# Performance work log

Measured on AMD Instinct MI355X. Metric: run time of the kernel, lower is better.

Reference implementation:

```python
import math
import jax, jax.numpy as jnp
import numpy as np

B, L, D, H = 4, 1024, 512, 8
DK = D // H

def setup_inputs() -> dict:
    key = jax.random.key(0)
    ks = jax.random.split(key, 12)
    s = 0.02
    return {
        "query": jax.random.normal(ks[0], (B, L, D), jnp.float32),
        "key": jax.random.normal(ks[1], (B, L, D), jnp.float32),
        "value": jax.random.normal(ks[2], (B, L, D), jnp.float32),
        "wq_w": jax.random.normal(ks[3], (D, D), jnp.float32) * s,
        "wq_b": jnp.zeros((D,), jnp.float32),
        "wk_w": jax.random.normal(ks[4], (D, D), jnp.float32) * s,
        "wk_b": jnp.zeros((D,), jnp.float32),
        "wv_w": jax.random.normal(ks[5], (D, D), jnp.float32) * s,
        "wv_b": jnp.zeros((D,), jnp.float32),
        "dense_w": jax.random.normal(ks[6], (D, D), jnp.float32) * s,
        "dense_b": jnp.zeros((D,), jnp.float32),
        "gate_w": jax.random.normal(ks[7], (D, 1), jnp.float32) * s,
        "gate_b": jnp.zeros((1,), jnp.float32),
        "mp_wq_w": jax.random.normal(ks[8], (D, D), jnp.float32) * s,
        "mp_wq_b": jnp.zeros((D,), jnp.float32),
        "mp_wk_w": jax.random.normal(ks[9], (D, D), jnp.float32) * s,
        "mp_wk_b": jnp.zeros((D,), jnp.float32),
    }

def reference(query, key, value, wq_w, wq_b, wk_w, wk_b, wv_w, wv_b,
              dense_w, dense_b, gate_w, gate_b,
              mp_wq_w, mp_wq_b, mp_wk_w, mp_wk_b):
    # Multi-head projections -> (B, H, L, DK)
    q = (query @ wq_w + wq_b).reshape(B, L, H, DK).transpose(0, 2, 1, 3)
    k = (key @ wk_w + wk_b).reshape(B, L, H, DK).transpose(0, 2, 1, 3)
    v = (value @ wv_w + wv_b).reshape(B, L, H, DK).transpose(0, 2, 1, 3)

    # MaskPerturbation on original (unprojected-into-heads) Q, K; scale by sqrt(d_model)
    qp = query @ mp_wq_w + mp_wq_b              # (B, L, D)
    kp = key @ mp_wk_w + mp_wk_b                # (B, L, D)
    m = jax.nn.sigmoid(jnp.einsum('bqd,bkd->bqk', qp, kp) / math.sqrt(D))  # (B, L, L)

    # Scaled dot-product attention (no mask)
    scores = jnp.einsum('bhqd,bhkd->bhqk', q, k) / math.sqrt(DK)  # (B, H, L, L)
    p_attn = jax.nn.softmax(scores, axis=-1)

    # Calibration: attn_cal = attn * exp(1 - m), combined with per-query gate, re-softmax
    attn_cal = p_attn * jnp.exp(1.0 - m[:, None])                 # (B, H, L, L)
    g = jax.nn.sigmoid(query @ gate_w + gate_b)[:, None]          # (B, 1, L, 1)
    attn_comb = g * p_attn + (1.0 - g) * attn_cal
    attn_final = jax.nn.softmax(attn_comb, axis=-1)

    out = jnp.einsum('bhqk,bhkd->bhqd', attn_final, v)            # (B, H, L, DK)
    out = out.transpose(0, 2, 1, 3).reshape(B, L, D)
    out = out @ dense_w + dense_b                                 # dropout p=0 (eval)
    return (out, m)
```

## Files before the change

### kernel.cpp

```cpp
#include <hip/hip_runtime.h>

#define B_  4
#define L_  1024
#define D_  512
#define H_  8
#define DK_ 64
#define BL_ (B_*L_)

typedef unsigned short us16;
typedef __attribute__((ext_vector_type(8))) short bf16x8;
typedef __attribute__((ext_vector_type(4))) float f32x4;

__device__ __forceinline__ float us2f(us16 u) {
  union { unsigned int i; float f; } x;
  x.i = ((unsigned int)u) << 16;
  return x.f;
}
__device__ __forceinline__ us16 f2us(float f) {
  union { float f; unsigned int i; } x;
  x.f = f;
  unsigned int r = x.i + 0x7FFFu + ((x.i >> 16) & 1u);
  return (us16)(r >> 16);
}
__device__ __forceinline__ us16 cvt_us(float f) { return f2us(f); }
__device__ __forceinline__ us16 cvt_us(us16 u) { return u; }
__device__ __forceinline__ float fexp2(float x) {
  return __builtin_amdgcn_exp2f(x);
}

#define MFMA(a, b, c) __builtin_amdgcn_mfma_f32_16x16x32_bf16(a, b, c, 0, 0, 0)

struct WT6 {
  const float* src[6];
  us16* dst[6];
};
__global__ __launch_bounds__(256) void wtrans6(WT6 p) {
  __shared__ us16 T[64][72];
  const int z = blockIdx.z;
  const float* __restrict__ W = p.src[z];
  us16* __restrict__ Wt = p.dst[z];
  const int t = threadIdx.x;
  const int k0 = blockIdx.y * 64, n0 = blockIdx.x * 64;
  {
    int r = t >> 2, c = (t & 3) * 16;
    const float* src = W + (size_t)(k0 + r) * 512 + n0 + c;
    union { bf16x8 v; us16 u[8]; } p0, p1;
#pragma unroll
    for (int j = 0; j < 8; ++j) { p0.u[j] = f2us(src[j]); p1.u[j] = f2us(src[8 + j]); }
    *(bf16x8*)&T[r][c] = p0.v;
    *(bf16x8*)&T[r][c + 8] = p1.v;
  }
  __syncthreads();
  {
    int n = t >> 2, c = (t & 3) * 16;
    union { bf16x8 v; us16 u[8]; } p0, p1;
#pragma unroll
    for (int j = 0; j < 8; ++j) { p0.u[j] = T[c + j][n]; p1.u[j] = T[c + 8 + j][n]; }
    us16* dst = Wt + (size_t)(n0 + n) * 512 + k0 + c;
    *(bf16x8*)dst = p0.v;
    *(bf16x8*)(dst + 8) = p1.v;
  }
}

struct GJob { const float* A; const us16* Wt; const float* bias; us16* C; int mode; };
struct GJobs { GJob j[3]; };

__global__ __launch_bounds__(256) void gemm3(GJobs jobs) {
  __shared__ us16 Al[64][72];
  __shared__ us16 Wl[64][72];
  int f = blockIdx.x + 8 * (blockIdx.y + 64 * blockIdx.z);
  const int cpx = 64 * (int)gridDim.z;
  f = (f & 7) * cpx + (f >> 3);
  const int bx = f & 7, by = (f >> 3) & 63, bz = f >> 9;
  const GJob J = jobs.j[bz];
  const int tid = threadIdx.x;
  const int w = tid >> 6, lane = tid & 63;
  const int quad = lane >> 4, lc = lane & 15;
  const int row0 = by * 64, col0 = bx * 64;
  const int sr = tid >> 2, sc = (tid & 3) * 16;
  f32x4 acc[4] = {};
  for (int k0 = 0; k0 < 512; k0 += 64) {
    {
      const float* as = J.A + (size_t)(row0 + sr) * 512 + k0 + sc;
      union { bf16x8 v; us16 u[8]; } p0, p1;
#pragma unroll
      for (int j = 0; j < 8; ++j) { p0.u[j] = f2us(as[j]); p1.u[j] = f2us(as[8 + j]); }
      *(bf16x8*)&Al[sr][sc] = p0.v;
      *(bf16x8*)&Al[sr][sc + 8] = p1.v;
    }
    {
      const us16* wsrc = J.Wt + (size_t)(col0 + sr) * 512 + k0 + sc;
      *(bf16x8*)&Wl[sr][sc] = *(const bf16x8*)wsrc;
      *(bf16x8*)&Wl[sr][sc + 8] = *(const bf16x8*)(wsrc + 8);
    }
    __syncthreads();
    bf16x8 a0 = *(const bf16x8*)&Al[w * 16 + lc][quad * 8];
    bf16x8 a1 = *(const bf16x8*)&Al[w * 16 + lc][32 + quad * 8];
#pragma unroll
    for (int ct = 0; ct < 4; ++ct) {
      bf16x8 b0 = *(const bf16x8*)&Wl[ct * 16 + lc][quad * 8];
      bf16x8 b1 = *(const bf16x8*)&Wl[ct * 16 + lc][32 + quad * 8];
      acc[ct] = MFMA(a0, b0, acc[ct]);
      acc[ct] = MFMA(a1, b1, acc[ct]);
    }
    __syncthreads();
  }
  const int orow = row0 + w * 16 + quad * 4;
#pragma unroll
  for (int ct = 0; ct < 4; ++ct) {
    const int col = col0 + ct * 16 + lc;
    const float bv = J.bias[col];
    if (J.mode == 0) {
#pragma unroll
      for (int r = 0; r < 4; ++r)
        J.C[(size_t)(orow + r) * 512 + col] = f2us(acc[ct][r] + bv);
    } else {
      const int h = col >> 6, dk = col & 63;
#pragma unroll
      for (int r = 0; r < 4; ++r) {
        const int grow = orow + r;
        const int b = grow >> 10, kv = grow & 1023;
        J.C[(((size_t)b * H_ + h) * DK_ + dk) * L_ + kv] = f2us(acc[ct][r] + bv);
      }
    }
  }
}

__global__ __launch_bounds__(256) void gemm_dense(
    const us16* __restrict__ A, const us16* __restrict__ Wt,
    const float* __restrict__ bias, float* __restrict__ C) {
  __shared__ us16 Al[64][72];
  __shared__ us16 Wl[64][72];
  int f = blockIdx.x + 8 * blockIdx.y;
  f = (f & 7) * 64 + (f >> 3);
  const int bx = f & 7, by = f >> 3;
  const int tid = threadIdx.x;
  const int w = tid >> 6, lane = tid & 63;
  const int quad = lane >> 4, lc = lane & 15;
  const int row0 = by * 64, col0 = bx * 64;
  const int sr = tid >> 2, sc = (tid & 3) * 16;
  f32x4 acc[4] = {};
  for (int k0 = 0; k0 < 512; k0 += 64) {
    const us16* as = A + (size_t)(row0 + sr) * 512 + k0 + sc;
    const us16* wsrc = Wt + (size_t)(col0 + sr) * 512 + k0 + sc;
    *(bf16x8*)&Al[sr][sc] = *(const bf16x8*)as;
    *(bf16x8*)&Al[sr][sc + 8] = *(const bf16x8*)(as + 8);
    *(bf16x8*)&Wl[sr][sc] = *(const bf16x8*)wsrc;
    *(bf16x8*)&Wl[sr][sc + 8] = *(const bf16x8*)(wsrc + 8);
    __syncthreads();
    bf16x8 a0 = *(const bf16x8*)&Al[w * 16 + lc][quad * 8];
    bf16x8 a1 = *(const bf16x8*)&Al[w * 16 + lc][32 + quad * 8];
#pragma unroll
    for (int ct = 0; ct < 4; ++ct) {
      bf16x8 b0 = *(const bf16x8*)&Wl[ct * 16 + lc][quad * 8];
      bf16x8 b1 = *(const bf16x8*)&Wl[ct * 16 + lc][32 + quad * 8];
      acc[ct] = MFMA(a0, b0, acc[ct]);
      acc[ct] = MFMA(a1, b1, acc[ct]);
    }
    __syncthreads();
  }
  const int orow = row0 + w * 16 + quad * 4;
#pragma unroll
  for (int ct = 0; ct < 4; ++ct) {
    const int col = col0 + ct * 16 + lc;
    const float bv = bias[col];
#pragma unroll
    for (int r = 0; r < 4; ++r)
      C[(size_t)(orow + r) * 512 + col] = acc[ct][r] + bv;
  }
}

__global__ __launch_bounds__(256) void gate_kernel(
    const float* __restrict__ query, const float* __restrict__ gw,
    const float* __restrict__ gb, float* __restrict__ g) {
  int row = blockIdx.x * 4 + (threadIdx.x >> 6);
  int lane = threadIdx.x & 63;
  float p = 0.f;
  for (int d = lane; d < D_; d += 64) p += query[(size_t)row * D_ + d] * gw[d];
#pragma unroll
  for (int off = 32; off; off >>= 1) p += __shfl_down(p, off);
  if (lane == 0) g[row] = 1.f / (1.f + __expf(-(p + gb[0])));
}

template <bool WK>
__global__ __launch_bounds__(256) void mask16(
    const us16* __restrict__ QP, const us16* __restrict__ KP,
    float* __restrict__ Mout, const float* __restrict__ gbuf,
    us16* __restrict__ Wk) {
  __shared__ us16 Al[64][56];
  __shared__ us16 Bl[64][56];
  int f = blockIdx.x + 16 * (blockIdx.y + 16 * blockIdx.z);
  f = (f & 7) * 128 + (f >> 3);
  const int bx = f & 15, by = (f >> 4) & 15, b = f >> 8;
  const int tid = threadIdx.x;
  const int w = tid >> 6, lane = tid & 63;
  const int quad = lane >> 4, lc = lane & 15;
  const int row0 = by * 64, col0 = bx * 64;
  const us16* Ab = QP + (size_t)b * L_ * D_;
  const us16* Bb = KP + (size_t)b * L_ * D_;
  f32x4 acc[4] = {};
  const int arow = tid >> 2, aks = (tid & 3) * 8;
  for (int k0 = 0; k0 < 512; k0 += 32) {
    *(bf16x8*)&Al[arow][aks] =
        *(const bf16x8*)(Ab + (size_t)(row0 + arow) * 512 + k0 + aks);
    *(bf16x8*)&Bl[arow][aks] =
        *(const bf16x8*)(Bb + (size_t)(col0 + arow) * 512 + k0 + aks);
    __syncthreads();
    bf16x8 af = *(const bf16x8*)&Al[w * 16 + lc][quad * 8];
#pragma unroll
    for (int ct = 0; ct < 4; ++ct) {
      bf16x8 bf = *(const bf16x8*)&Bl[ct * 16 + lc][quad * 8];
      acc[ct] = MFMA(af, bf, acc[ct]);
    }
    __syncthreads();
  }
  const float sc = 0.04419417382415922f;
  const int orow = row0 + w * 16 + quad * 4;
  float gq[4];
  if (WK) {
#pragma unroll
    for (int r = 0; r < 4; ++r) gq[r] = gbuf[b * L_ + orow + r];
  }
#pragma unroll
  for (int ct = 0; ct < 4; ++ct) {
    const int col = col0 + ct * 16 + lc;
#pragma unroll
    for (int r = 0; r < 4; ++r) {
      float x = acc[ct][r] * sc;
      float v = 1.f / (1.f + __expf(-x));
      size_t idx = ((size_t)b * L_ + orow + r) * L_ + col;
      Mout[idx] = v;
      if (WK) Wk[idx] = f2us(gq[r] + (1.f - gq[r]) * __expf(1.f - v));
    }
  }
}

__global__ __launch_bounds__(256, 4) void attn5(
    const us16* Qp, const us16* __restrict__ Kp,
    const us16* __restrict__ Vt, const us16* __restrict__ Wk, us16* O) {
  __shared__ us16 P[16 * 1032];
  __shared__ float red[2][4][16];
  const int tid = threadIdx.x;
  const int w = tid >> 6, lane = tid & 63;
  const int quad = lane >> 4, lc = lane & 15;
  int f = blockIdx.x + 64 * (blockIdx.y + 8 * blockIdx.z);
  f = (f & 7) * 256 + (f >> 3);
  const int q0 = (f & 63) * 16;
  const int h = (f >> 6) & 7;
  const int b = f >> 9;

  const us16* qptr = Qp + (size_t)(b * L_ + q0 + lc) * D_ + h * DK_;
  bf16x8 qa0 = *(const bf16x8*)(qptr + quad * 8);
  bf16x8 qa1 = *(const bf16x8*)(qptr + 32 + quad * 8);

  const us16* Kbase = Kp + (size_t)b * L_ * D_ + h * DK_;
  const float c1 = 0.18033688011112042f;

  float s[16][4];
  float sm[4] = {0.f, 0.f, 0.f, 0.f};
#pragma unroll
  for (int kt = 0; kt < 16; ++kt) {
    const us16* kr = Kbase + (size_t)(kt * 64 + w * 16 + lc) * D_;
    bf16x8 b0 = *(const bf16x8*)(kr + quad * 8);
    bf16x8 b1 = *(const bf16x8*)(kr + 32 + quad * 8);
    f32x4 a = {};
    __builtin_amdgcn_s_setprio(1);
    a = MFMA(qa0, b0, a);
    a = MFMA(qa1, b1, a);
    __builtin_amdgcn_s_setprio(0);
#pragma unroll
    for (int r = 0; r < 4; ++r) {
      float e = fexp2(a[r] * c1);
      s[kt][r] = e;
      sm[r] += e;
    }
  }
#pragma unroll
  for (int r = 0; r < 4; ++r)
#pragma unroll
    for (int off = 1; off < 16; off <<= 1) sm[r] += __shfl_xor(sm[r], off);
  if (lc == 0)
#pragma unroll
    for (int r = 0; r < 4; ++r) red[0][w][quad * 4 + r] = sm[r];
  __syncthreads();
  float invr[4];
#pragma unroll
  for (int r = 0; r < 4; ++r) {
    const int row = quad * 4 + r;
    invr[r] = 1.44269504088896341f /
              (red[0][0][row] + red[0][1][row] + red[0][2][row] + red[0][3][row]);
  }

  const us16* wkb = Wk + (size_t)(b * L_ + q0 + quad * 4) * L_ + w * 16 + lc;
  float ts[4] = {0.f, 0.f, 0.f, 0.f};
#pragma unroll
  for (int kt = 0; kt < 16; ++kt) {
#pragma unroll
    for (int r = 0; r < 4; ++r) {
      float cv = s[kt][r] * invr[r] * us2f(wkb[(size_t)r * L_ + kt * 64]);
      float e2 = fexp2(cv);
      ts[r] += e2;
      P[(quad * 4 + r) * 1032 + kt * 64 + w * 16 + lc] = f2us(e2);
    }
  }
#pragma unroll
  for (int r = 0; r < 4; ++r)
#pragma unroll
    for (int off = 1; off < 16; off <<= 1) ts[r] += __shfl_xor(ts[r], off);
  if (lc == 0)
#pragma unroll
    for (int r = 0; r < 4; ++r) red[1][w][quad * 4 + r] = ts[r];
  __syncthreads();

  const us16* Vb = Vt + ((size_t)(b * H_ + h) * DK_ + w * 16 + lc) * L_;
  f32x4 oacc = {};
  for (int kv = 0; kv < L_; kv += 32) {
    bf16x8 pa = *(const bf16x8*)&P[lc * 1032 + kv + quad * 8];
    bf16x8 vb = *(const bf16x8*)(Vb + kv + quad * 8);
    __builtin_amdgcn_s_setprio(1);
    oacc = MFMA(pa, vb, oacc);
    __builtin_amdgcn_s_setprio(0);
  }
#pragma unroll
  for (int r = 0; r < 4; ++r) {
    const int row = quad * 4 + r;
    float inv2 = 1.f /
        (red[1][0][row] + red[1][1][row] + red[1][2][row] + red[1][3][row]);
    O[(size_t)(b * L_ + q0 + row) * D_ + h * DK_ + w * 16 + lc] =
        f2us(oacc[r] * inv2);
  }
}

template <int MODE, typename TA>
__global__ __launch_bounds__(256) void gemm16(
    const TA* __restrict__ A, const float* __restrict__ W,
    const float* __restrict__ bias, void* __restrict__ Cout) {
  __shared__ us16 Al[64][56];
  __shared__ us16 Wl[64][56];
  const int tid = threadIdx.x;
  const int w = tid >> 6, lane = tid & 63;
  const int quad = lane >> 4, lc = lane & 15;
  const int row0 = blockIdx.y * 64, col0 = blockIdx.x * 64;
  f32x4 acc[4] = {};
  const int arow = tid >> 2, aks = (tid & 3) * 8;
  const int wk = tid & 31, wns = (tid >> 5) * 8;
  for (int k0 = 0; k0 < 512; k0 += 32) {
    {
      union { bf16x8 v; us16 u[8]; } pk;
      const TA* src = A + (size_t)(row0 + arow) * 512 + k0 + aks;
#pragma unroll
      for (int j = 0; j < 8; ++j) pk.u[j] = cvt_us(src[j]);
      *(bf16x8*)&Al[arow][aks] = pk.v;
    }
    {
      const float* src = W + (size_t)(k0 + wk) * 512 + col0 + wns;
#pragma unroll
      for (int j = 0; j < 8; ++j) Wl[wns + j][wk] = f2us(src[j]);
    }
    __syncthreads();
    bf16x8 af = *(const bf16x8*)&Al[w * 16 + lc][quad * 8];
#pragma unroll
    for (int ct = 0; ct < 4; ++ct) {
      bf16x8 bf = *(const bf16x8*)&Wl[ct * 16 + lc][quad * 8];
      acc[ct] = MFMA(af, bf, acc[ct]);
    }
    __syncthreads();
  }
  const int orow = row0 + w * 16 + quad * 4;
#pragma unroll
  for (int ct = 0; ct < 4; ++ct) {
    const int col = col0 + ct * 16 + lc;
    const float bv = bias[col];
    if (MODE == 0) {
      us16* C = (us16*)Cout;
#pragma unroll
      for (int r = 0; r < 4; ++r)
        C[(size_t)(orow + r) * 512 + col] = f2us(acc[ct][r] + bv);
    } else if (MODE == 1) {
      us16* C = (us16*)Cout;
      const int h = col >> 6, dk = col & 63;
#pragma unroll
      for (int r = 0; r < 4; ++r) {
        const int grow = orow + r;
        const int b = grow >> 10, kv = grow & 1023;
        C[(((size_t)b * H_ + h) * DK_ + dk) * L_ + kv] = f2us(acc[ct][r] + bv);
      }
    } else {
      float* C = (float*)Cout;
#pragma unroll
      for (int r = 0; r < 4; ++r)
        C[(size_t)(orow + r) * 512 + col] = acc[ct][r] + bv;
    }
  }
}

__global__ __launch_bounds__(256, 3) void attn2_fb(
    const us16* Qp, const us16* __restrict__ Kp,
    const us16* __restrict__ Vt, const float* __restrict__ Mm,
    const float* __restrict__ gbuf, us16* O) {
  __shared__ us16 Ql[16][72];
  __shared__ us16 P[16 * 1032];
  __shared__ float red[2][4][16];
  const int tid = threadIdx.x;
  const int w = tid >> 6, lane = tid & 63;
  const int quad = lane >> 4, lc = lane & 15;
  const int b = blockIdx.z, h = blockIdx.y, q0 = blockIdx.x * 16;
  if (tid < 128) {
    int r = tid >> 3, ks = (tid & 7) * 8;
    *(bf16x8*)&Ql[r][ks] =
        *(const bf16x8*)(Qp + (size_t)(b * L_ + q0 + r) * D_ + h * DK_ + ks);
  }
  __syncthreads();
  bf16x8 qa0 = *(const bf16x8*)&Ql[lc][quad * 8];
  bf16x8 qa1 = *(const bf16x8*)&Ql[lc][32 + quad * 8];
  const us16* Kbase = Kp + (size_t)b * L_ * D_ + h * DK_;
  float s[16][4];
#pragma unroll
  for (int kt = 0; kt < 16; ++kt) {
    const us16* kr = Kbase + (size_t)(kt * 64 + w * 16 + lc) * D_;
    bf16x8 b0 = *(const bf16x8*)(kr + quad * 8);
    bf16x8 b1 = *(const bf16x8*)(kr + 32 + quad * 8);
    f32x4 a = {};
    a = MFMA(qa0, b0, a);
    a = MFMA(qa1, b1, a);
#pragma unroll
    for (int r = 0; r < 4; ++r) s[kt][r] = a[r] * 0.125f;
  }
  float sm[4];
#pragma unroll
  for (int r = 0; r < 4; ++r) {
    float t = 0.f;
#pragma unroll
    for (int kt = 0; kt < 16; ++kt) { s[kt][r] = __expf(s[kt][r]); t += s[kt][r]; }
#pragma unroll
    for (int off = 1; off < 16; off <<= 1) t += __shfl_xor(t, off);
    sm[r] = t;
  }
  if (lc == 0)
#pragma unroll
    for (int r = 0; r < 4; ++r) red[0][w][quad * 4 + r] = sm[r];
  __syncthreads();
  float inv[4];
#pragma unroll
  for (int r = 0; r < 4; ++r) {
    const int row = quad * 4 + r;
    inv[r] = 1.f / (red[0][0][row] + red[0][1][row] + red[0][2][row] + red[0][3][row]);
  }
  float gq[4];
#pragma unroll
  for (int r = 0; r < 4; ++r) gq[r] = gbuf[b * L_ + q0 + quad * 4 + r];
#pragma unroll
  for (int r = 0; r < 4; ++r) {
    const float* mrow = Mm + (size_t)(b * L_ + q0 + quad * 4 + r) * L_;
    float t = 0.f;
#pragma unroll
    for (int kt = 0; kt < 16; ++kt) {
      float mval = mrow[kt * 64 + w * 16 + lc];
      float c = s[kt][r] * inv[r] * (gq[r] + (1.f - gq[r]) * __expf(1.f - mval));
      float e = __expf(c);
      s[kt][r] = e;
      t += e;
    }
#pragma unroll
    for (int off = 1; off < 16; off <<= 1) t += __shfl_xor(t, off);
    sm[r] = t;
  }
  if (lc == 0)
#pragma unroll
    for (int r = 0; r < 4; ++r) red[1][w][quad * 4 + r] = sm[r];
  __syncthreads();
#pragma unroll
  for (int r = 0; r < 4; ++r) {
    const int row = quad * 4 + r;
    inv[r] = 1.f / (red[1][0][row] + red[1][1][row] + red[1][2][row] + red[1][3][row]);
  }
#pragma unroll
  for (int kt = 0; kt < 16; ++kt)
#pragma unroll
    for (int r = 0; r < 4; ++r)
      P[(quad * 4 + r) * 1032 + kt * 64 + w * 16 + lc] = f2us(s[kt][r] * inv[r]);
  __syncthreads();
  const us16* Vb = Vt + (size_t)(b * H_ + h) * DK_ * L_;
  f32x4 oacc = {};
  for (int kv = 0; kv < L_; kv += 32) {
    bf16x8 pa = *(const bf16x8*)&P[lc * 1032 + kv + quad * 8];
    bf16x8 vb = *(const bf16x8*)(Vb + (size_t)(w * 16 + lc) * L_ + kv + quad * 8);
    oacc = MFMA(pa, vb, oacc);
  }
#pragma unroll
  for (int r = 0; r < 4; ++r)
    O[(size_t)(b * L_ + q0 + quad * 4 + r) * D_ + h * DK_ + w * 16 + lc] =
        f2us(oacc[r]);
}

extern "C" void kernel_launch(void* const* d_in, const int* in_sizes, int n_in,
                              void* d_out, int out_size, void* d_ws, size_t ws_size,
                              hipStream_t stream) {
  const float* query   = (const float*)d_in[0];
  const float* key     = (const float*)d_in[1];
  const float* value   = (const float*)d_in[2];
  const float* wq_w    = (const float*)d_in[3];
  const float* wq_b    = (const float*)d_in[4];
  const float* wk_w    = (const float*)d_in[5];
  const float* wk_b    = (const float*)d_in[6];
  const float* wv_w    = (const float*)d_in[7];
  const float* wv_b    = (const float*)d_in[8];
  const float* dense_w = (const float*)d_in[9];
  const float* dense_b = (const float*)d_in[10];
  const float* gate_w  = (const float*)d_in[11];
  const float* gate_b  = (const float*)d_in[12];
  const float* mp_wq_w = (const float*)d_in[13];
  const float* mp_wq_b = (const float*)d_in[14];
  const float* mp_wk_w = (const float*)d_in[15];
  const float* mp_wk_b = (const float*)d_in[16];

  const size_t RSZ = (size_t)BL_ * D_;
  const size_t WSZ = (size_t)D_ * D_;
  us16* R0 = (us16*)d_ws;
  us16* R1 = R0 + RSZ;

  float* out0 = (float*)d_out;
  float* outm = out0 + (size_t)B_ * L_ * D_;
  us16*  Vt   = (us16*)d_out;
  float* gbuf = (float*)((char*)d_out + (4u << 20));

  dim3 blk(256);
  dim3 gattn(L_ / 16, H_, B_);

  if (ws_size >= ((size_t)20 << 20)) {
    us16* Wt0 = R1 + RSZ;
    us16* mpq_t = Wt0;
    us16* mpk_t = Wt0 + WSZ;
    us16* wq_t  = Wt0 + 2 * WSZ;
    us16* wk_t  = Wt0 + 3 * WSZ;
    us16* wv_t  = Wt0 + 4 * WSZ;
    us16* dw_t  = Wt0 + 5 * WSZ;
    us16* Wk    = Wt0 + 6 * WSZ;

    WT6 wt;
    wt.src[0] = mp_wq_w; wt.dst[0] = mpq_t;
    wt.src[1] = mp_wk_w; wt.dst[1] = mpk_t;
    wt.src[2] = wq_w;    wt.dst[2] = wq_t;
    wt.src[3] = wk_w;    wt.dst[3] = wk_t;
    wt.src[4] = wv_w;    wt.dst[4] = wv_t;
    wt.src[5] = dense_w; wt.dst[5] = dw_t;
    hipLaunchKernelGGL(wtrans6, dim3(8, 8, 6), blk, 0, stream, wt);
    hipLaunchKernelGGL(gate_kernel, dim3(BL_ / 4), blk, 0, stream, query, gate_w, gate_b, gbuf);

    GJobs mp;
    mp.j[0] = { query, mpq_t, mp_wq_b, R0, 0 };
    mp.j[1] = { key,   mpk_t, mp_wk_b, R1, 0 };
    mp.j[2] = mp.j[1];
    hipLaunchKernelGGL(gemm3, dim3(8, 64, 2), blk, 0, stream, mp);
    hipLaunchKernelGGL(mask16<true>, dim3(16, 16, B_), blk, 0, stream,
                       R0, R1, outm, gbuf, Wk);

    GJobs qkv;
    qkv.j[0] = { query, wq_t, wq_b, R0, 0 };
    qkv.j[1] = { key,   wk_t, wk_b, R1, 0 };
    qkv.j[2] = { value, wv_t, wv_b, Vt, 1 };
    hipLaunchKernelGGL(gemm3, dim3(8, 64, 3), blk, 0, stream, qkv);

    hipLaunchKernelGGL(attn5, gattn, blk, 0, stream, R0, R1, Vt, Wk, R0);
    hipLaunchKernelGGL(gemm_dense, dim3(8, 64), blk, 0, stream, R0, dw_t, dense_b, out0);
  } else {
    dim3 gproj(8, 64);
    hipLaunchKernelGGL((gemm16<0, float>), gproj, blk, 0, stream, query, mp_wq_w, mp_wq_b, (void*)R0);
    hipLaunchKernelGGL((gemm16<0, float>), gproj, blk, 0, stream, key,   mp_wk_w, mp_wk_b, (void*)R1);
    hipLaunchKernelGGL(mask16<false>, dim3(16, 16, B_), blk, 0, stream,
                       R0, R1, outm, (const float*)nullptr, (us16*)nullptr);
    hipLaunchKernelGGL((gemm16<0, float>), gproj, blk, 0, stream, query, wq_w, wq_b, (void*)R0);
    hipLaunchKernelGGL((gemm16<0, float>), gproj, blk, 0, stream, key,   wk_w, wk_b, (void*)R1);
    hipLaunchKernelGGL((gemm16<1, float>), gproj, blk, 0, stream, value, wv_w, wv_b, (void*)Vt);
    hipLaunchKernelGGL(gate_kernel, dim3(BL_ / 4), blk, 0, stream, query, gate_w, gate_b, gbuf);
    hipLaunchKernelGGL(attn2_fb, gattn, blk, 0, stream, R0, R1, Vt, outm, gbuf, R0);
    hipLaunchKernelGGL((gemm16<2, us16>), gproj, blk, 0, stream, R0, dense_w, dense_b, (void*)out0);
  }
}
```

Before: 240.0 us.

## Fuse prep kernels, pre-convert query to bf16, widen mask K-tile, remap attention blocks

```diff
diff --git a/kernel.cpp b/kernel.cpp
--- a/kernel.cpp
+++ b/kernel.cpp
@@ -34,13 +34,37 @@
   const float* src[6];
   us16* dst[6];
 };
-__global__ __launch_bounds__(256) void wtrans6(WT6 p) {
+__global__ __launch_bounds__(256) void prep(WT6 p, const float* __restrict__ query,
+    const float* __restrict__ gw, const float* __restrict__ gb,
+    float* __restrict__ g, us16* __restrict__ qb) {
   __shared__ us16 T[64][72];
-  const int z = blockIdx.z;
+  int id = blockIdx.x;
+  const int t = threadIdx.x;
+  if (id < 1024) {
+    int row = id * 4 + (t >> 6);
+    int lane = t & 63;
+    float pz = 0.f;
+    for (int d = lane; d < D_; d += 64) pz += query[(size_t)row * D_ + d] * gw[d];
+#pragma unroll
+    for (int off = 32; off; off >>= 1) pz += __shfl_down(pz, off);
+    if (lane == 0) g[row] = 1.f / (1.f + __expf(-(pz + gb[0])));
+    return;
+  }
+  if (id >= 1408) {
+    size_t base = (size_t)(id - 1408) * 4096 + t * 16;
+    const float* src = query + base;
+    union { bf16x8 v; us16 u[8]; } a0, a1;
+#pragma unroll
+    for (int j = 0; j < 8; ++j) { a0.u[j] = f2us(src[j]); a1.u[j] = f2us(src[8 + j]); }
+    *(bf16x8*)&qb[base] = a0.v;
+    *(bf16x8*)&qb[base + 8] = a1.v;
+    return;
+  }
+  id -= 1024;
+  const int z = id >> 6;
+  const int k0 = ((id >> 3) & 7) * 64, n0 = (id & 7) * 64;
   const float* __restrict__ W = p.src[z];
   us16* __restrict__ Wt = p.dst[z];
-  const int t = threadIdx.x;
-  const int k0 = blockIdx.y * 64, n0 = blockIdx.x * 64;
   {
     int r = t >> 2, c = (t & 3) * 16;
     const float* src = W + (size_t)(k0 + r) * 512 + n0 + c;
@@ -62,7 +86,22 @@
   }
 }
 
-struct GJob { const float* A; const us16* Wt; const float* bias; us16* C; int mode; };
+__global__ __launch_bounds__(256) void gate_kernel(
+    const float* __restrict__ query, const float* __restrict__ gw,
+    const float* __restrict__ gb, float* __restrict__ g) {
+  int row = blockIdx.x * 4 + (threadIdx.x >> 6);
+  int lane = threadIdx.x & 63;
+  float p = 0.f;
+  for (int d = lane; d < D_; d += 64) p += query[(size_t)row * D_ + d] * gw[d];
+#pragma unroll
+  for (int off = 32; off; off >>= 1) p += __shfl_down(p, off);
+  if (lane == 0) g[row] = 1.f / (1.f + __expf(-(p + gb[0])));
+}
+
+struct GJob {
+  const float* A; const us16* Ab; const us16* Wt;
+  const float* bias; us16* C; int mode; int atype;
+};
 struct GJobs { GJob j[3]; };
 
 __global__ __launch_bounds__(256) void gemm3(GJobs jobs) {
@@ -80,7 +119,11 @@
   const int sr = tid >> 2, sc = (tid & 3) * 16;
   f32x4 acc[4] = {};
   for (int k0 = 0; k0 < 512; k0 += 64) {
-    {
+    if (J.atype) {
+      const us16* as = J.Ab + (size_t)(row0 + sr) * 512 + k0 + sc;
+      *(bf16x8*)&Al[sr][sc] = *(const bf16x8*)as;
+      *(bf16x8*)&Al[sr][sc + 8] = *(const bf16x8*)(as + 8);
+    } else {
       const float* as = J.A + (size_t)(row0 + sr) * 512 + k0 + sc;
       union { bf16x8 v; us16 u[8]; } p0, p1;
 #pragma unroll
@@ -170,25 +213,13 @@
   }
 }
 
-__global__ __launch_bounds__(256) void gate_kernel(
-    const float* __restrict__ query, const float* __restrict__ gw,
-    const float* __restrict__ gb, float* __restrict__ g) {
-  int row = blockIdx.x * 4 + (threadIdx.x >> 6);
-  int lane = threadIdx.x & 63;
-  float p = 0.f;
-  for (int d = lane; d < D_; d += 64) p += query[(size_t)row * D_ + d] * gw[d];
-#pragma unroll
-  for (int off = 32; off; off >>= 1) p += __shfl_down(p, off);
-  if (lane == 0) g[row] = 1.f / (1.f + __expf(-(p + gb[0])));
-}
-
 template <bool WK>
 __global__ __launch_bounds__(256) void mask16(
     const us16* __restrict__ QP, const us16* __restrict__ KP,
     float* __restrict__ Mout, const float* __restrict__ gbuf,
     us16* __restrict__ Wk) {
-  __shared__ us16 Al[64][56];
-  __shared__ us16 Bl[64][56];
+  __shared__ us16 Al[64][72];
+  __shared__ us16 Bl[64][72];
   int f = blockIdx.x + 16 * (blockIdx.y + 16 * blockIdx.z);
   f = (f & 7) * 128 + (f >> 3);
   const int bx = f & 15, by = (f >> 4) & 15, b = f >> 8;
@@ -198,23 +229,32 @@
   const int row0 = by * 64, col0 = bx * 64;
   const us16* Ab = QP + (size_t)b * L_ * D_;
   const us16* Bb = KP + (size_t)b * L_ * D_;
+  const int sr = tid >> 2, sc = (tid & 3) * 16;
   f32x4 acc[4] = {};
-  const int arow = tid >> 2, aks = (tid & 3) * 8;
-  for (int k0 = 0; k0 < 512; k0 += 32) {
-    *(bf16x8*)&Al[arow][aks] =
-        *(const bf16x8*)(Ab + (size_t)(row0 + arow) * 512 + k0 + aks);
-    *(bf16x8*)&Bl[arow][aks] =
-        *(const bf16x8*)(Bb + (size_t)(col0 + arow) * 512 + k0 + aks);
-    __syncthreads();
-    bf16x8 af = *(const bf16x8*)&Al[w * 16 + lc][quad * 8];
+  for (int k0 = 0; k0 < 512; k0 += 64) {
+    {
+      const us16* as = Ab + (size_t)(row0 + sr) * 512 + k0 + sc;
+      *(bf16x8*)&Al[sr][sc] = *(const bf16x8*)as;
+      *(bf16x8*)&Al[sr][sc + 8] = *(const bf16x8*)(as + 8);
+    }
+    {
+      const us16* bs = Bb + (size_t)(col0 + sr) * 512 + k0 + sc;
+      *(bf16x8*)&Bl[sr][sc] = *(const bf16x8*)bs;
+      *(bf16x8*)&Bl[sr][sc + 8] = *(const bf16x8*)(bs + 8);
+    }
+    __syncthreads();
+    bf16x8 a0 = *(const bf16x8*)&Al[w * 16 + lc][quad * 8];
+    bf16x8 a1 = *(const bf16x8*)&Al[w * 16 + lc][32 + quad * 8];
 #pragma unroll
     for (int ct = 0; ct < 4; ++ct) {
-      bf16x8 bf = *(const bf16x8*)&Bl[ct * 16 + lc][quad * 8];
-      acc[ct] = MFMA(af, bf, acc[ct]);
-    }
-    __syncthreads();
-  }
-  const float sc = 0.04419417382415922f;
+      bf16x8 b0 = *(const bf16x8*)&Bl[ct * 16 + lc][quad * 8];
+      bf16x8 b1 = *(const bf16x8*)&Bl[ct * 16 + lc][32 + quad * 8];
+      acc[ct] = MFMA(a0, b0, acc[ct]);
+      acc[ct] = MFMA(a1, b1, acc[ct]);
+    }
+    __syncthreads();
+  }
+  const float sc2 = 0.04419417382415922f;
   const int orow = row0 + w * 16 + quad * 4;
   float gq[4];
   if (WK) {
@@ -226,7 +266,7 @@
     const int col = col0 + ct * 16 + lc;
 #pragma unroll
     for (int r = 0; r < 4; ++r) {
-      float x = acc[ct][r] * sc;
+      float x = acc[ct][r] * sc2;
       float v = 1.f / (1.f + __expf(-x));
       size_t idx = ((size_t)b * L_ + orow + r) * L_ + col;
       Mout[idx] = v;
@@ -243,11 +283,12 @@
   const int tid = threadIdx.x;
   const int w = tid >> 6, lane = tid & 63;
   const int quad = lane >> 4, lc = lane & 15;
-  int f = blockIdx.x + 64 * (blockIdx.y + 8 * blockIdx.z);
-  f = (f & 7) * 256 + (f >> 3);
-  const int q0 = (f & 63) * 16;
-  const int h = (f >> 6) & 7;
-  const int b = f >> 9;
+  int raw = blockIdx.x + 64 * (blockIdx.y + 8 * blockIdx.z);
+  const int c = raw & 7;
+  const int rest = raw >> 3;
+  const int gg = c * 4 + (rest & 3);
+  const int q0 = (rest >> 2) * 16;
+  const int h = gg & 7, b = gg >> 3;
 
   const us16* qptr = Qp + (size_t)(b * L_ + q0 + lc) * D_ + h * DK_;
   bf16x8 qa0 = *(const bf16x8*)(qptr + quad * 8);
@@ -522,10 +563,8 @@
   float* out0 = (float*)d_out;
   float* outm = out0 + (size_t)B_ * L_ * D_;
   us16*  Vt   = (us16*)d_out;
-  float* gbuf = (float*)((char*)d_out + (4u << 20));
 
   dim3 blk(256);
-  dim3 gattn(L_ / 16, H_, B_);
 
   if (ws_size >= ((size_t)20 << 20)) {
     us16* Wt0 = R1 + RSZ;
@@ -536,6 +575,8 @@
     us16* wv_t  = Wt0 + 4 * WSZ;
     us16* dw_t  = Wt0 + 5 * WSZ;
     us16* Wk    = Wt0 + 6 * WSZ;
+    float* gbuf = (float*)(Wk + (size_t)B_ * L_ * L_);
+    us16* qb = (us16*)((char*)d_out + (4u << 20));
 
     WT6 wt;
     wt.src[0] = mp_wq_w; wt.dst[0] = mpq_t;
@@ -544,26 +585,26 @@
     wt.src[3] = wk_w;    wt.dst[3] = wk_t;
     wt.src[4] = wv_w;    wt.dst[4] = wv_t;
     wt.src[5] = dense_w; wt.dst[5] = dw_t;
-    hipLaunchKernelGGL(wtrans6, dim3(8, 8, 6), blk, 0, stream, wt);
-    hipLaunchKernelGGL(gate_kernel, dim3(BL_ / 4), blk, 0, stream, query, gate_w, gate_b, gbuf);
+    hipLaunchKernelGGL(prep, dim3(1920), blk, 0, stream, wt, query, gate_w, gate_b, gbuf, qb);
 
     GJobs mp;
-    mp.j[0] = { query, mpq_t, mp_wq_b, R0, 0 };
-    mp.j[1] = { key,   mpk_t, mp_wk_b, R1, 0 };
+    mp.j[0] = { nullptr, qb, mpq_t, mp_wq_b, R0, 0, 1 };
+    mp.j[1] = { key, nullptr, mpk_t, mp_wk_b, R1, 0, 0 };
     mp.j[2] = mp.j[1];
     hipLaunchKernelGGL(gemm3, dim3(8, 64, 2), blk, 0, stream, mp);
     hipLaunchKernelGGL(mask16<true>, dim3(16, 16, B_), blk, 0, stream,
                        R0, R1, outm, gbuf, Wk);
 
     GJobs qkv;
-    qkv.j[0] = { query, wq_t, wq_b, R0, 0 };
-    qkv.j[1] = { key,   wk_t, wk_b, R1, 0 };
-    qkv.j[2] = { value, wv_t, wv_b, Vt, 1 };
+    qkv.j[0] = { nullptr, qb, wq_t, wq_b, R0, 0, 1 };
+    qkv.j[1] = { key, nullptr, wk_t, wk_b, R1, 0, 0 };
+    qkv.j[2] = { value, nullptr, wv_t, wv_b, Vt, 1, 0 };
     hipLaunchKernelGGL(gemm3, dim3(8, 64, 3), blk, 0, stream, qkv);
 
-    hipLaunchKernelGGL(attn5, gattn, blk, 0, stream, R0, R1, Vt, Wk, R0);
+    hipLaunchKernelGGL(attn5, dim3(L_ / 16, H_, B_), blk, 0, stream, R0, R1, Vt, Wk, R0);
     hipLaunchKernelGGL(gemm_dense, dim3(8, 64), blk, 0, stream, R0, dw_t, dense_b, out0);
   } else {
+    float* gbuf = (float*)((char*)d_out + (4u << 20));
     dim3 gproj(8, 64);
     hipLaunchKernelGGL((gemm16<0, float>), gproj, blk, 0, stream, query, mp_wq_w, mp_wq_b, (void*)R0);
     hipLaunchKernelGGL((gemm16<0, float>), gproj, blk, 0, stream, key,   mp_wk_w, mp_wk_b, (void*)R1);
@@ -573,7 +614,7 @@
     hipLaunchKernelGGL((gemm16<0, float>), gproj, blk, 0, stream, key,   wk_w, wk_b, (void*)R1);
     hipLaunchKernelGGL((gemm16<1, float>), gproj, blk, 0, stream, value, wv_w, wv_b, (void*)Vt);
     hipLaunchKernelGGL(gate_kernel, dim3(BL_ / 4), blk, 0, stream, query, gate_w, gate_b, gbuf);
-    hipLaunchKernelGGL(attn2_fb, gattn, blk, 0, stream, R0, R1, Vt, outm, gbuf, R0);
+    hipLaunchKernelGGL(attn2_fb, dim3(L_ / 16, H_, B_), blk, 0, stream, R0, R1, Vt, outm, gbuf, R0);
     hipLaunchKernelGGL((gemm16<2, us16>), gproj, blk, 0, stream, R0, dense_w, dense_b, (void*)out0);
   }
 }
```

After: 241.4 us. About the same (+0.6%).
